# Performance work log

Hardware: AMD Instinct MI355X
Metric: run time of the kernel (lower is better)

Reference implementation:

```python
import jax, jax.numpy as jnp
import numpy as np

EPS = 1e-8  # torch F.cosine_similarity eps


def setup_inputs() -> dict:
    key = jax.random.key(0)
    ks = jax.random.split(key, 10)
    S, B, V, D, H = 512, 128, 50257, 300, 512
    return {
        "context": jax.random.randint(ks[0], (32, B), 0, V),
        "ends": jax.random.randint(ks[1], (S, B), 0, V),
        "ends_ls": jax.random.randint(ks[2], (B,), 0, S),
        "embed_mat": jax.random.normal(ks[3], (V, D), jnp.float32),
        "w_ih": jax.random.normal(ks[4], (3 * H, 1), jnp.float32) * 0.05,
        "w_hh": jax.random.normal(ks[5], (3 * H, H), jnp.float32) * 0.05,
        "b_ih": jax.random.normal(ks[6], (3 * H,), jnp.float32) * 0.05,
        "b_hh": jax.random.normal(ks[7], (3 * H,), jnp.float32) * 0.05,
        "fc_w": jax.random.normal(ks[8], (1, H), jnp.float32) * 0.05,
        "fc_b": jax.random.normal(ks[9], (1,), jnp.float32) * 0.05,
    }


def _rep_features(embeds):
    # embeds: [S, B, D]. Causal max cosine similarity per position/batch.
    S = embeds.shape[0]
    norms = jnp.linalg.norm(embeds, axis=-1, keepdims=True)  # [S,B,1]
    xn = embeds / jnp.maximum(norms, EPS)
    sims = jnp.einsum("ibd,jbd->ijb", xn, xn)  # [S,S,B]
    sims = jnp.where(jnp.isnan(sims), -1.0, sims)  # sims[sims != sims] = -1
    i = jnp.arange(S)[:, None]
    j = jnp.arange(S)[None, :]
    causal = (j < i)[:, :, None]  # strictly past positions
    sims = jnp.where(causal, sims, -jnp.inf)
    feats = jnp.max(sims, axis=1)  # [S,B]
    feats = feats.at[0].set(0.0)  # position 0 -> zeros
    return feats


def _gru(x_seq, w_ih, w_hh, b_ih, b_hh, h0):
    # x_seq: [S, B, 1]; returns final hidden state [B, H]
    H = h0.shape[-1]

    def step(h, x):
        gi = x @ w_ih.T + b_ih  # [B, 3H]
        gh = h @ w_hh.T + b_hh
        ir, iz, inn = gi[:, :H], gi[:, H:2 * H], gi[:, 2 * H:]
        hr, hz, hn = gh[:, :H], gh[:, H:2 * H], gh[:, 2 * H:]
        r = jax.nn.sigmoid(ir + hr)
        z = jax.nn.sigmoid(iz + hz)
        n = jnp.tanh(inn + r * hn)
        h_new = (1.0 - z) * n + z * h
        return h_new, None

    h_last, _ = jax.lax.scan(step, h0, x_seq)
    return h_last


def reference(context, ends, ends_ls, embed_mat, w_ih, w_hh, b_ih, b_hh, fc_w, fc_b):
    S, B = ends.shape
    embeds = embed_mat[ends.reshape(-1)].reshape(S, B, -1)  # [S,B,D]
    feats = _rep_features(embeds)[:, :, None]  # [S,B,1]
    h0 = jnp.zeros((B, w_hh.shape[-1]), feats.dtype)
    h_last = _gru(feats, w_ih, w_hh, b_ih, b_hh, h0)  # [B,H]
    final = (h_last @ fc_w.T + fc_b).reshape(-1)  # [B]
    return final
```

## Files before the change

### kernel.cpp

```cpp
#include <hip/hip_runtime.h>
#include <hip/hip_bf16.h>
#include <math.h>

#define S_LEN 512
#define B_N   128
#define D_EMB 300
#define KP    320
#define H_N   512

typedef __attribute__((ext_vector_type(8)))  short short8;
typedef __attribute__((ext_vector_type(8)))  unsigned short ushort8;
typedef __attribute__((ext_vector_type(4)))  unsigned int uint4v;
typedef __attribute__((ext_vector_type(4)))  float float4v;
typedef __attribute__((ext_vector_type(16))) float float16v;

__device__ __forceinline__ unsigned short f32_to_bf16(float f) {
  unsigned u = __float_as_uint(f);
  u = (u + 0x7fffu + ((u >> 16) & 1u)) >> 16;
  return (unsigned short)u;
}
__device__ __forceinline__ float bf16_to_f32(unsigned short h) {
  return __uint_as_float(((unsigned)h) << 16);
}
__device__ __forceinline__ short8 as_short8(uint4v v) {
  union { uint4v u; short8 s; } c; c.u = v; return c.s;
}

__global__ __launch_bounds__(256) void k1_embed_norm(
    const int* __restrict__ ends, const float* __restrict__ emb,
    unsigned short* __restrict__ xh, unsigned short* __restrict__ xl) {
  int wave = threadIdx.x >> 6, lane = threadIdx.x & 63;
  int vec = blockIdx.x * 4 + wave;
  int b = vec & (B_N - 1), s = vec >> 7;
  int v = ends[vec];
  const float* row = emb + (size_t)v * D_EMB;
  float e0 = row[lane], e1 = row[lane + 64], e2 = row[lane + 128], e3 = row[lane + 192];
  float e4 = (lane + 256 < D_EMB) ? row[lane + 256] : 0.f;
  float ss = e0*e0 + e1*e1 + e2*e2 + e3*e3 + e4*e4;
  #pragma unroll
  for (int m = 1; m < 64; m <<= 1) ss += __shfl_xor(ss, m);
  float sc = 1.0f / fmaxf(sqrtf(ss), 1e-8f);
  size_t base = ((size_t)b * S_LEN + s) * KP;
  float xs[5] = { e0*sc, e1*sc, e2*sc, e3*sc, (lane + 256 < D_EMB) ? e4*sc : 0.f };
  #pragma unroll
  for (int i = 0; i < 5; ++i) {
    unsigned short hi = f32_to_bf16(xs[i]);
    unsigned short lo = f32_to_bf16(xs[i] - bf16_to_f32(hi));
    xh[base + lane + 64*i] = hi;
    xl[base + lane + 64*i] = lo;
  }
}

#define KC  80
#define LDP 88

__global__ __launch_bounds__(256) void k2_feats(
    const unsigned short* __restrict__ xh, const unsigned short* __restrict__ xl,
    float* __restrict__ feats) {
  __shared__ __align__(16) unsigned short sBh[2][64*LDP], sBl[2][64*LDP];
  __shared__ float rbuf[4][32];
  int b   = blockIdx.x;
  int ic  = 7 - blockIdx.y;
  int tid = threadIdx.x;
  int wave = tid >> 6, lane = tid & 63;
  int itl = wave & 1, jtl = wave >> 1;
  int itg = ic * 2 + itl;
  size_t xbase = (size_t)b * S_LEN * KP;
  int arow0 = ic * 64;
  const size_t arowoff = xbase + (size_t)(arow0 + itl * 32 + (lane & 31)) * KP
                       + (size_t)((lane >> 5) * 8);

  short8 a_h[4][5], a_l[4][5];
  #pragma unroll
  for (int kc = 0; kc < 4; ++kc) {
    #pragma unroll
    for (int ks = 0; ks < 5; ++ks) {
      size_t ga = arowoff + kc * KC + ks * 16;
      a_h[kc][ks] = *(const short8*)&xh[ga];
      a_l[kc][ks] = *(const short8*)&xl[ga];
    }
  }

  float rm[16];
  #pragma unroll
  for (int r = 0; r < 16; ++r) rm[r] = -INFINITY;

  for (int u = tid; u < 640; u += 256) {
    int r = u / 10, sg = u % 10;
    size_t gb = xbase + (size_t)r * KP + sg * 8;
    int la = r * LDP + sg * 8;
    *(ushort8*)&sBh[0][la] = *(const ushort8*)&xh[gb];
    *(ushort8*)&sBl[0][la] = *(const ushort8*)&xl[gb];
  }
  __syncthreads();

  int buf = 0;
  for (int jc = 0; jc <= ic; ++jc) {
    int jt = jc * 2 + jtl;
    bool active = (jt <= itg);
    float16v acc;
    #pragma unroll
    for (int r = 0; r < 16; ++r) acc[r] = 0.f;

    #pragma unroll
    for (int kc = 0; kc < 4; ++kc) {
      bool last = (jc == ic) && (kc == 3);
      if (!last) {
        int jn = (kc < 3) ? jc : jc + 1;
        int kn = (kc + 1) & 3;
        for (int u = tid; u < 640; u += 256) {
          int r = u / 10, sg = u % 10;
          size_t gb = xbase + (size_t)(jn * 64 + r) * KP + kn * KC + sg * 8;
          int la = r * LDP + sg * 8;
          *(ushort8*)&sBh[buf ^ 1][la] = *(const ushort8*)&xh[gb];
          *(ushort8*)&sBl[buf ^ 1][la] = *(const ushort8*)&xl[gb];
        }
      }
      if (active) {
        int br = (jtl * 32 + (lane & 31)) * LDP;
        int kq = (lane >> 5) * 8;
        #pragma unroll
        for (int ks = 0; ks < 5; ++ks) {
          short8 b_h = *(const short8*)&sBh[buf][br + ks*16 + kq];
          short8 b_l = *(const short8*)&sBl[buf][br + ks*16 + kq];
          acc = __builtin_amdgcn_mfma_f32_32x32x16_bf16(a_h[kc][ks], b_h, acc, 0, 0, 0);
          acc = __builtin_amdgcn_mfma_f32_32x32x16_bf16(a_h[kc][ks], b_l, acc, 0, 0, 0);
          acc = __builtin_amdgcn_mfma_f32_32x32x16_bf16(a_l[kc][ks], b_h, acc, 0, 0, 0);
        }
      }
      __syncthreads();
      buf ^= 1;
    }
    if (active) {
      int colg = jt * 32 + (lane & 31);
      #pragma unroll
      for (int r = 0; r < 16; ++r) {
        int rowg = itg * 32 + (r & 3) + 8*(r >> 2) + 4*(lane >> 5);
        float v = acc[r];
        if (jt == itg && colg >= rowg) v = -INFINITY;
        rm[r] = fmaxf(rm[r], v);
      }
    }
  }
  #pragma unroll
  for (int r = 0; r < 16; ++r) {
    float v = rm[r];
    v = fmaxf(v, __shfl_xor(v, 1));
    v = fmaxf(v, __shfl_xor(v, 2));
    v = fmaxf(v, __shfl_xor(v, 4));
    v = fmaxf(v, __shfl_xor(v, 8));
    v = fmaxf(v, __shfl_xor(v, 16));
    rm[r] = v;
  }
  if ((lane & 31) == 0) {
    int half = lane >> 5;
    #pragma unroll
    for (int r = 0; r < 16; ++r)
      rbuf[wave][(r & 3) + 8*(r >> 2) + 4*half] = rm[r];
  }
  __syncthreads();
  if (tid < 64) {
    int it2 = tid >> 5, rl = tid & 31;
    float v = fmaxf(rbuf[it2][rl], rbuf[it2 + 2][rl]);
    int i = ic * 64 + it2 * 32 + rl;
    feats[i * B_N + b] = (i == 0) ? 0.0f : v;
  }
}

#define HW64 (B_N * H_N / 2)

__global__ __launch_bounds__(512, 1) void k3_gru(
    const float* __restrict__ feats,
    const float* __restrict__ w_ih, const float* __restrict__ w_hh,
    const float* __restrict__ b_ih, const float* __restrict__ b_hh,
    const float* __restrict__ fc_w, const float* __restrict__ fc_b,
    unsigned long long* __restrict__ hq, unsigned int* __restrict__ bars,
    float* __restrict__ out) {
  __shared__ __align__(16) float4v red2[8][16][16];
  __shared__ float osum[256];
  int tid = threadIdx.x;
  int wave = tid >> 6, lane = tid & 63;
  int g = blockIdx.x & 7, s = blockIdx.x >> 3;

  short8 wfh[3][2], wfl[3][2];
  {
    int nloc = lane & 15;
    int kq = (lane >> 4) * 8;
    #pragma unroll
    for (int gt = 0; gt < 3; ++gt) {
      const float* wr = w_hh + (size_t)(gt * H_N + s * 16 + nloc) * H_N;
      #pragma unroll
      for (int ks = 0; ks < 2; ++ks) {
        int k0 = wave * 64 + ks * 32 + kq;
        short8 h8, l8;
        #pragma unroll
        for (int j = 0; j < 8; ++j) {
          float wv = wr[k0 + j];
          unsigned short hi = f32_to_bf16(wv);
          unsigned short lo = f32_to_bf16(wv - bf16_to_f32(hi));
          h8[j] = (short)hi; l8[j] = (short)lo;
        }
        wfh[gt][ks] = h8; wfl[gt][ks] = l8;
      }
    }
  }
  const bool gater = (tid < 256);
  int bb = tid >> 4, jj = tid & 15;
  int jr = s * 16 + jj;
  float wihr = w_ih[jr], wihz = w_ih[H_N + jr], wihn = w_ih[2*H_N + jr];
  float bir = b_ih[jr],  biz = b_ih[H_N + jr],  bin_ = b_ih[2*H_N + jr];
  float bhr = b_hh[jr],  bhz = b_hh[H_N + jr],  bhn = b_hh[2*H_N + jr];
  float fcw = fc_w[jr];
  int gb = g * 16 + (bb & 15);
  float h_old = 0.f;
  const unsigned int* fp = bars + g * 32 + wave * 4 + (lane & 3);
  unsigned int* myflag = bars + g * 32 + s;

  const int Cp = g * 16 + (s >> 3) * 4 + ((s >> 1) & 3);
  const int qp = (2 * s + (jj >> 3)) & 3;
  const size_t prodoff = (size_t)Cp * 512 + (size_t)qp * 128 + (size_t)(bb & 15) * 8;
  const size_t cbase = (size_t)(g * 16 + wave * 2) * 512 + (size_t)lane * 8;

  for (int t = 0; t < S_LEN; ++t) {
    float x = gater ? feats[t * B_N + gb] : 0.f;
    float sr = 0.f, sz = 0.f, sn = 0.f;
    if (t > 0) {
      {
        const unsigned tgt = (unsigned)t;
        for (;;) {
          unsigned f = __hip_atomic_load(fp, __ATOMIC_RELAXED, __HIP_MEMORY_SCOPE_AGENT);
          if (__ballot(f < tgt) == 0ull) break;
        }
        asm volatile("" ::: "memory");
      }
      const unsigned short* hh =
          (const unsigned short*)(hq + (size_t)((t - 1) & 1) * HW64);
      const unsigned short* hbase = hh + cbase;
      const unsigned short* lbase = hbase + 65536;
      uint4v rh0, rh1, rl0, rl1;
      asm volatile(
        "global_load_dwordx4 %0, %4, off sc1\n\t"
        "global_load_dwordx4 %1, %4, off offset:1024 sc1\n\t"
        "global_load_dwordx4 %2, %5, off sc1\n\t"
        "global_load_dwordx4 %3, %5, off offset:1024 sc1\n\t"
        "s_waitcnt vmcnt(0)"
        : "=&v"(rh0), "=&v"(rh1), "=&v"(rl0), "=&v"(rl1)
        : "v"(hbase), "v"(lbase)
        : "memory");
      short8 ah0 = as_short8(rh0), ah1 = as_short8(rh1);
      short8 al0 = as_short8(rl0), al1 = as_short8(rl1);
      float4v a0, a1, a2;
      #pragma unroll
      for (int r = 0; r < 4; ++r) { a0[r] = 0.f; a1[r] = 0.f; a2[r] = 0.f; }
      a0 = __builtin_amdgcn_mfma_f32_16x16x32_bf16(ah0, wfh[0][0], a0, 0,0,0);
      a1 = __builtin_amdgcn_mfma_f32_16x16x32_bf16(ah0, wfh[1][0], a1, 0,0,0);
      a2 = __builtin_amdgcn_mfma_f32_16x16x32_bf16(ah0, wfh[2][0], a2, 0,0,0);
      a0 = __builtin_amdgcn_mfma_f32_16x16x32_bf16(ah0, wfl[0][0], a0, 0,0,0);
      a1 = __builtin_amdgcn_mfma_f32_16x16x32_bf16(ah0, wfl[1][0], a1, 0,0,0);
      a2 = __builtin_amdgcn_mfma_f32_16x16x32_bf16(ah0, wfl[2][0], a2, 0,0,0);
      a0 = __builtin_amdgcn_mfma_f32_16x16x32_bf16(al0, wfh[0][0], a0, 0,0,0);
      a1 = __builtin_amdgcn_mfma_f32_16x16x32_bf16(al0, wfh[1][0], a1, 0,0,0);
      a2 = __builtin_amdgcn_mfma_f32_16x16x32_bf16(al0, wfh[2][0], a2, 0,0,0);
      a0 = __builtin_amdgcn_mfma_f32_16x16x32_bf16(ah1, wfh[0][1], a0, 0,0,0);
      a1 = __builtin_amdgcn_mfma_f32_16x16x32_bf16(ah1, wfh[1][1], a1, 0,0,0);
      a2 = __builtin_amdgcn_mfma_f32_16x16x32_bf16(ah1, wfh[2][1], a2, 0,0,0);
      a0 = __builtin_amdgcn_mfma_f32_16x16x32_bf16(ah1, wfl[0][1], a0, 0,0,0);
      a1 = __builtin_amdgcn_mfma_f32_16x16x32_bf16(ah1, wfl[1][1], a1, 0,0,0);
      a2 = __builtin_amdgcn_mfma_f32_16x16x32_bf16(ah1, wfl[2][1], a2, 0,0,0);
      a0 = __builtin_amdgcn_mfma_f32_16x16x32_bf16(al1, wfh[0][1], a0, 0,0,0);
      a1 = __builtin_amdgcn_mfma_f32_16x16x32_bf16(al1, wfh[1][1], a1, 0,0,0);
      a2 = __builtin_amdgcn_mfma_f32_16x16x32_bf16(al1, wfh[2][1], a2, 0,0,0);
      int colw = lane & 15, roww = (lane >> 4) * 4;
      #pragma unroll
      for (int r = 0; r < 4; ++r) {
        float4v w; w[0] = a0[r]; w[1] = a1[r]; w[2] = a2[r]; w[3] = 0.f;
        red2[wave][roww + r][colw] = w;
      }
      __syncthreads();
      if (gater) {
        float4v sv = red2[0][bb][jj];
        #pragma unroll
        for (int w8 = 1; w8 < 8; ++w8) sv += red2[w8][bb][jj];
        sr = sv[0]; sz = sv[1]; sn = sv[2];
      }
    }
    if (gater) {
      float ar_ = fminf(fmaxf(x * wihr + bir + sr + bhr, -30.f), 30.f);
      float az_ = fminf(fmaxf(x * wihz + biz + sz + bhz, -30.f), 30.f);
      float r_ = __builtin_amdgcn_rcpf(1.f + __expf(-ar_));
      float z_ = __builtin_amdgcn_rcpf(1.f + __expf(-az_));
      float an_ = fminf(fmaxf(x * wihn + bin_ + r_ * (sn + bhn), -30.f), 30.f);
      float en = __expf(-2.f * an_);
      float n_ = (1.f - en) * __builtin_amdgcn_rcpf(1.f + en);
      float h_new = (1.f - z_) * n_ + z_ * h_old;
      h_old = h_new;
      if (t < S_LEN - 1) {
        unsigned short hi16 = f32_to_bf16(h_new);
        unsigned short lo16 = f32_to_bf16(h_new - bf16_to_f32(hi16));
        unsigned myh = hi16, myl = lo16;
        unsigned oh = (unsigned)__shfl_xor((int)myh, 1);
        unsigned ol = (unsigned)__shfl_xor((int)myl, 1);
        bool od1 = (jj & 1) != 0;
        unsigned pH = od1 ? (oh | (myh << 16)) : (myh | (oh << 16));
        unsigned pL = od1 ? (ol | (myl << 16)) : (myl | (ol << 16));
        unsigned qh = (unsigned)__shfl_xor((int)pH, 2);
        unsigned ql = (unsigned)__shfl_xor((int)pL, 2);
        bool od2 = (jj & 2) != 0;
        unsigned h01 = od2 ? qh : pH, h23 = od2 ? pH : qh;
        unsigned l01 = od2 ? ql : pL, l23 = od2 ? pL : ql;
        unsigned xh01 = (unsigned)__shfl_xor((int)h01, 4);
        unsigned xh23 = (unsigned)__shfl_xor((int)h23, 4);
        unsigned xl01 = (unsigned)__shfl_xor((int)l01, 4);
        unsigned xl23 = (unsigned)__shfl_xor((int)l23, 4);
        bool od4 = (jj & 4) != 0;
        uint4v runH, runL;
        runH[0] = od4 ? xh01 : h01; runH[1] = od4 ? xh23 : h23;
        runH[2] = od4 ? h01 : xh01; runH[3] = od4 ? h23 : xh23;
        runL[0] = od4 ? xl01 : l01; runL[1] = od4 ? xl23 : l23;
        runL[2] = od4 ? l01 : xl01; runL[3] = od4 ? l23 : xl23;
        unsigned short* hh = (unsigned short*)(hq + (size_t)(t & 1) * HW64);
        if ((jj & 3) == 0) {
          if ((jj & 4) == 0) *(uint4v*)(hh + prodoff)         = runH;
          else               *(uint4v*)(hh + 65536 + prodoff) = runL;
        }
      }
    }
    if (t < S_LEN - 1) {
      asm volatile("s_waitcnt vmcnt(0)" ::: "memory");
      __syncthreads();
      if (tid == 0)
        __hip_atomic_store(myflag, (unsigned)(t + 1),
                           __ATOMIC_RELAXED, __HIP_MEMORY_SCOPE_WORKGROUP);
    }
  }
  if (gater) osum[tid] = h_old * fcw;
  __syncthreads();
  if (gater && jj == 0) {
    float acc = 0.f;
    #pragma unroll
    for (int q = 0; q < 16; ++q) acc += osum[bb * 16 + q];
    if (s == 0) acc += fc_b[0];
    atomicAdd(&out[gb], acc);
  }
}

extern "C" void kernel_launch(void* const* d_in, const int* in_sizes, int n_in,
                              void* d_out, int out_size, void* d_ws, size_t ws_size,
                              hipStream_t stream) {
  (void)in_sizes; (void)n_in; (void)out_size; (void)ws_size;
  const int*   ends = (const int*)d_in[1];
  const float* emb  = (const float*)d_in[3];
  const float* w_ih = (const float*)d_in[4];
  const float* w_hh = (const float*)d_in[5];
  const float* b_ih = (const float*)d_in[6];
  const float* b_hh = (const float*)d_in[7];
  const float* fc_w = (const float*)d_in[8];
  const float* fc_b = (const float*)d_in[9];
  float* out = (float*)d_out;

  size_t xn_elems = (size_t)B_N * S_LEN * KP;
  unsigned short* xh = (unsigned short*)d_ws;
  unsigned short* xl = xh + xn_elems;
  float* feats = (float*)(xl + xn_elems);
  unsigned long long* hq = (unsigned long long*)(feats + S_LEN * B_N);
  unsigned int* bars = (unsigned int*)(hq + 2 * (size_t)HW64);

  hipMemsetAsync(out, 0, sizeof(float) * B_N, stream);
  hipMemsetAsync(bars, 0, 4096, stream);

  k1_embed_norm<<<dim3(S_LEN * B_N / 4), dim3(256), 0, stream>>>(ends, emb, xh, xl);
  k2_feats<<<dim3(B_N, 8), dim3(256), 0, stream>>>(xh, xl, feats);

  void* args[] = { (void*)&feats, (void*)&w_ih, (void*)&w_hh, (void*)&b_ih,
                   (void*)&b_hh, (void*)&fc_w, (void*)&fc_b,
                   (void*)&hq, (void*)&bars, (void*)&out };
  hipLaunchCooperativeKernel((void*)k3_gru, dim3(256), dim3(512), args, 0, stream);
}
```

Baseline: 1.032 ms.

## Enlarge k2 row tile to 128 rows per block and add sleep in GRU spin-wait

The similarity kernel now gives each wave its own 32-row A tile (128 rows per block) and has each wave compute both 32-column B subtiles of every staged 64-row chunk. Each LDS-staged B tile is therefore reused by four row tiles instead of two, and the grid is halved. The cross-wave reduction through shared memory and the extra barrier are removed, and each wave writes feats directly. Separately, the GRU barrier spin loop gets an s_sleep to reduce polling pressure, which may add some wake-up latency on each of the 512 steps.

```diff
diff --git a/kernel.cpp b/kernel.cpp
--- a/kernel.cpp
+++ b/kernel.cpp
@@ -58,16 +58,13 @@
     const unsigned short* __restrict__ xh, const unsigned short* __restrict__ xl,
     float* __restrict__ feats) {
   __shared__ __align__(16) unsigned short sBh[2][64*LDP], sBl[2][64*LDP];
-  __shared__ float rbuf[4][32];
   int b   = blockIdx.x;
-  int ic  = 7 - blockIdx.y;
+  int ic2 = 3 - blockIdx.y;
   int tid = threadIdx.x;
   int wave = tid >> 6, lane = tid & 63;
-  int itl = wave & 1, jtl = wave >> 1;
-  int itg = ic * 2 + itl;
+  int itg = ic2 * 4 + wave;
   size_t xbase = (size_t)b * S_LEN * KP;
-  int arow0 = ic * 64;
-  const size_t arowoff = xbase + (size_t)(arow0 + itl * 32 + (lane & 31)) * KP
+  const size_t arowoff = xbase + (size_t)(itg * 32 + (lane & 31)) * KP
                        + (size_t)((lane >> 5) * 8);
 
   short8 a_h[4][5], a_l[4][5];
@@ -84,6 +81,8 @@
   float rm[16];
   #pragma unroll
   for (int r = 0; r < 16; ++r) rm[r] = -INFINITY;
+
+  const int NJ = 2 * ic2 + 2;
 
   for (int u = tid; u < 640; u += 256) {
     int r = u / 10, sg = u % 10;
@@ -95,16 +94,16 @@
   __syncthreads();
 
   int buf = 0;
-  for (int jc = 0; jc <= ic; ++jc) {
-    int jt = jc * 2 + jtl;
-    bool active = (jt <= itg);
-    float16v acc;
-    #pragma unroll
-    for (int r = 0; r < 16; ++r) acc[r] = 0.f;
+  for (int jc = 0; jc < NJ; ++jc) {
+    int jt0 = jc * 2, jt1 = jc * 2 + 1;
+    bool act0 = (jt0 <= itg), act1 = (jt1 <= itg);
+    float16v acc0, acc1;
+    #pragma unroll
+    for (int r = 0; r < 16; ++r) { acc0[r] = 0.f; acc1[r] = 0.f; }
 
     #pragma unroll
     for (int kc = 0; kc < 4; ++kc) {
-      bool last = (jc == ic) && (kc == 3);
+      bool last = (jc == NJ - 1) && (kc == 3);
       if (!last) {
         int jn = (kc < 3) ? jc : jc + 1;
         int kn = (kc + 1) & 3;
@@ -116,28 +115,49 @@
           *(ushort8*)&sBl[buf ^ 1][la] = *(const ushort8*)&xl[gb];
         }
       }
-      if (active) {
-        int br = (jtl * 32 + (lane & 31)) * LDP;
-        int kq = (lane >> 5) * 8;
+      int kq = (lane >> 5) * 8;
+      if (act0) {
+        int br = (lane & 31) * LDP;
         #pragma unroll
         for (int ks = 0; ks < 5; ++ks) {
           short8 b_h = *(const short8*)&sBh[buf][br + ks*16 + kq];
           short8 b_l = *(const short8*)&sBl[buf][br + ks*16 + kq];
-          acc = __builtin_amdgcn_mfma_f32_32x32x16_bf16(a_h[kc][ks], b_h, acc, 0, 0, 0);
-          acc = __builtin_amdgcn_mfma_f32_32x32x16_bf16(a_h[kc][ks], b_l, acc, 0, 0, 0);
-          acc = __builtin_amdgcn_mfma_f32_32x32x16_bf16(a_l[kc][ks], b_h, acc, 0, 0, 0);
+          acc0 = __builtin_amdgcn_mfma_f32_32x32x16_bf16(a_h[kc][ks], b_h, acc0, 0, 0, 0);
+          acc0 = __builtin_amdgcn_mfma_f32_32x32x16_bf16(a_h[kc][ks], b_l, acc0, 0, 0, 0);
+          acc0 = __builtin_amdgcn_mfma_f32_32x32x16_bf16(a_l[kc][ks], b_h, acc0, 0, 0, 0);
+        }
+      }
+      if (act1) {
+        int br = (32 + (lane & 31)) * LDP;
+        #pragma unroll
+        for (int ks = 0; ks < 5; ++ks) {
+          short8 b_h = *(const short8*)&sBh[buf][br + ks*16 + kq];
+          short8 b_l = *(const short8*)&sBl[buf][br + ks*16 + kq];
+          acc1 = __builtin_amdgcn_mfma_f32_32x32x16_bf16(a_h[kc][ks], b_h, acc1, 0, 0, 0);
+          acc1 = __builtin_amdgcn_mfma_f32_32x32x16_bf16(a_h[kc][ks], b_l, acc1, 0, 0, 0);
+          acc1 = __builtin_amdgcn_mfma_f32_32x32x16_bf16(a_l[kc][ks], b_h, acc1, 0, 0, 0);
         }
       }
       __syncthreads();
       buf ^= 1;
     }
-    if (active) {
-      int colg = jt * 32 + (lane & 31);
+    if (act0) {
+      int colg = jt0 * 32 + (lane & 31);
       #pragma unroll
       for (int r = 0; r < 16; ++r) {
         int rowg = itg * 32 + (r & 3) + 8*(r >> 2) + 4*(lane >> 5);
-        float v = acc[r];
-        if (jt == itg && colg >= rowg) v = -INFINITY;
+        float v = acc0[r];
+        if (jt0 == itg && colg >= rowg) v = -INFINITY;
+        rm[r] = fmaxf(rm[r], v);
+      }
+    }
+    if (act1) {
+      int colg = jt1 * 32 + (lane & 31);
+      #pragma unroll
+      for (int r = 0; r < 16; ++r) {
+        int rowg = itg * 32 + (r & 3) + 8*(r >> 2) + 4*(lane >> 5);
+        float v = acc1[r];
+        if (jt1 == itg && colg >= rowg) v = -INFINITY;
         rm[r] = fmaxf(rm[r], v);
       }
     }
@@ -155,15 +175,10 @@
   if ((lane & 31) == 0) {
     int half = lane >> 5;
     #pragma unroll
-    for (int r = 0; r < 16; ++r)
-      rbuf[wave][(r & 3) + 8*(r >> 2) + 4*half] = rm[r];
-  }
-  __syncthreads();
-  if (tid < 64) {
-    int it2 = tid >> 5, rl = tid & 31;
-    float v = fmaxf(rbuf[it2][rl], rbuf[it2 + 2][rl]);
-    int i = ic * 64 + it2 * 32 + rl;
-    feats[i * B_N + b] = (i == 0) ? 0.0f : v;
+    for (int r = 0; r < 16; ++r) {
+      int i = itg * 32 + (r & 3) + 8*(r >> 2) + 4*half;
+      feats[i * B_N + b] = (i == 0) ? 0.0f : rm[r];
+    }
   }
 }
 
@@ -230,6 +245,7 @@
         for (;;) {
           unsigned f = __hip_atomic_load(fp, __ATOMIC_RELAXED, __HIP_MEMORY_SCOPE_AGENT);
           if (__ballot(f < tgt) == 0ull) break;
+          __builtin_amdgcn_s_sleep(1);
         }
         asm volatile("" ::: "memory");
       }
@@ -369,7 +385,7 @@
   hipMemsetAsync(bars, 0, 4096, stream);
 
   k1_embed_norm<<<dim3(S_LEN * B_N / 4), dim3(256), 0, stream>>>(ends, emb, xh, xl);
-  k2_feats<<<dim3(B_N, 8), dim3(256), 0, stream>>>(xh, xl, feats);
+  k2_feats<<<dim3(B_N, 4), dim3(256), 0, stream>>>(xh, xl, feats);
 
   void* args[] = { (void*)&feats, (void*)&w_ih, (void*)&w_hh, (void*)&b_ih,
                    (void*)&b_hh, (void*)&fc_w, (void*)&fc_b,
```

New measurement: 1.026 ms. About the same (-0.6%).
